# Kernel optimization log

Measured on AMD Instinct MI355X. Metric: run time of the kernel, lower is better.

## Reference

```python
import jax, jax.numpy as jnp
import numpy as np

B, T, D = 2, 2048, 1024
F_DIM = 4096
E = 8


def setup_inputs() -> dict:
    key = jax.random.key(0)
    ks = jax.random.split(key, 6)
    x = jax.random.normal(ks[0], (B, T, D), dtype=jnp.float32)
    Wr = jax.random.normal(ks[1], (E, D), dtype=jnp.float32) * 0.02  # router weight [E, D]
    W1 = jax.random.normal(ks[2], (E, F_DIM, D), dtype=jnp.float32) * 0.02  # per-expert Linear(D->F) weights
    b1 = jnp.zeros((E, F_DIM), dtype=jnp.float32)
    W2 = jax.random.normal(ks[3], (E, D, F_DIM), dtype=jnp.float32) * 0.02  # per-expert Linear(F->D) weights
    b2 = jnp.zeros((E, D), dtype=jnp.float32)
    return {"x": x, "Wr": Wr, "W1": W1, "b1": b1, "W2": W2, "b2": b2, "top_k": 2}


def reference(x, Wr, W1, b1, W2, b2, top_k):
    # router scores: [b, t, E]
    scores = jnp.einsum('btd,ed->bte', x, Wr)
    topk_vals, topk_idx = jax.lax.top_k(scores, top_k)  # [b, t, k]
    # Dense compute over all experts (E is small); grouped-GEMM equivalent of the
    # original per-token loop. hidden: [b, t, E, F]
    h = jax.nn.relu(jnp.einsum('btd,efd->btef', x, W1) + b1)
    all_out = jnp.einsum('btef,edf->bted', h, W2) + b2  # [b, t, E, D]
    # gather the top-k experts' outputs per token: [b, t, k, D]
    gathered = jnp.take_along_axis(all_out, topk_idx[..., None], axis=2)
    # FAITHFUL to source: softmax over the sequence dim (dim=-1 of [b, t]),
    # applied independently per top-k slot.
    weight = jax.nn.softmax(topk_vals, axis=1)  # [b, t, k]
    out = jnp.sum(weight[..., None] * gathered, axis=2)  # [b, t, D]
    return out
```

## Files before the change

kernel.cpp:

```cpp
#include <hip/hip_runtime.h>
#include <stdint.h>

typedef short bf16x8 __attribute__((ext_vector_type(8)));
typedef float f32x4 __attribute__((ext_vector_type(4)));

#define NTOK 4096
#define DDIM 1024
#define FDIM 4096
#define NEXP 8
#define SEQ  2048

#define FB_MAXROWS 8704
#define FB_MAXTILES 136
#define N_MAXROWS 9216
#define N_MAXTILES 72

#define GLOAD16(g, l) __builtin_amdgcn_global_load_lds( \
    (const __attribute__((address_space(1))) unsigned int*)(const void*)(g), \
    (__attribute__((address_space(3))) unsigned int*)(l), 16, 0, 0)

__device__ __forceinline__ unsigned short f2bf(float f) {
    union { float f; unsigned int u; } v; v.f = f;
    unsigned int u = v.u;
    unsigned int r = (u + 0x7FFFu + ((u >> 16) & 1u)) >> 16;
    return (unsigned short)r;
}
__device__ __forceinline__ unsigned int pk2(float a, float b) {
    return (unsigned int)f2bf(a) | ((unsigned int)f2bf(b) << 16);
}

__global__ __launch_bounds__(256) void cvt_kernel(
    const float* __restrict__ src, unsigned short* __restrict__ dst, int n4)
{
    int i = blockIdx.x * 256 + threadIdx.x;
    const int stride = gridDim.x * 256;
    for (; i < n4; i += stride) {
        const float4 v = ((const float4*)src)[i];
        ushort4 o;
        o.x = f2bf(v.x); o.y = f2bf(v.y); o.z = f2bf(v.z); o.w = f2bf(v.w);
        ((ushort4*)dst)[i] = o;
    }
}

__global__ __launch_bounds__(256) void router_kernel(
    const float* __restrict__ x, const float* __restrict__ Wr,
    float* __restrict__ topk_vals, int* __restrict__ topk_idx,
    int* __restrict__ counts)
{
    const int wave = threadIdx.x >> 6;
    const int lane = threadIdx.x & 63;
    const int t = blockIdx.x * 4 + wave;
    const float4* xr = (const float4*)(x + (size_t)t * DDIM);

    float acc[NEXP];
#pragma unroll
    for (int e = 0; e < NEXP; ++e) acc[e] = 0.0f;

    for (int d = lane; d < DDIM / 4; d += 64) {
        const float4 xv = xr[d];
#pragma unroll
        for (int e = 0; e < NEXP; ++e) {
            const float4 wv = ((const float4*)(Wr + e * DDIM))[d];
            acc[e] = fmaf(xv.x, wv.x, acc[e]);
            acc[e] = fmaf(xv.y, wv.y, acc[e]);
            acc[e] = fmaf(xv.z, wv.z, acc[e]);
            acc[e] = fmaf(xv.w, wv.w, acc[e]);
        }
    }
#pragma unroll
    for (int e = 0; e < NEXP; ++e) {
        for (int off = 32; off > 0; off >>= 1)
            acc[e] += __shfl_xor(acc[e], off, 64);
    }
    if (lane == 0) {
        float best = -3.4e38f, second = -3.4e38f;
        int bi = 0, si = 0;
#pragma unroll
        for (int e = 0; e < NEXP; ++e) {
            const float s = acc[e];
            if (s > best) { second = best; si = bi; best = s; bi = e; }
            else if (s > second) { second = s; si = e; }
        }
        topk_vals[t * 2 + 0] = best;
        topk_vals[t * 2 + 1] = second;
        topk_idx[t * 2 + 0] = bi;
        topk_idx[t * 2 + 1] = si;
        atomicAdd(&counts[bi], 1);
        atomicAdd(&counts[si], 1);
    }
}

__global__ __launch_bounds__(256) void softmax_seq_kernel(
    const float* __restrict__ tv, float* __restrict__ weight)
{
    const int b = blockIdx.x >> 1;
    const int k = blockIdx.x & 1;
    const float* base = tv + (size_t)b * SEQ * 2 + k;
    float* wbase = weight + (size_t)b * SEQ * 2 + k;
    __shared__ float red[256];
    const int tid = threadIdx.x;

    float m = -3.4e38f;
    for (int t = tid; t < SEQ; t += 256) m = fmaxf(m, base[t * 2]);
    red[tid] = m; __syncthreads();
    for (int s = 128; s > 0; s >>= 1) {
        if (tid < s) red[tid] = fmaxf(red[tid], red[tid + s]);
        __syncthreads();
    }
    m = red[0];
    __syncthreads();

    float sum = 0.0f;
    for (int t = tid; t < SEQ; t += 256) sum += expf(base[t * 2] - m);
    red[tid] = sum; __syncthreads();
    for (int s = 128; s > 0; s >>= 1) {
        if (tid < s) red[tid] += red[tid + s];
        __syncthreads();
    }
    const float inv = 1.0f / red[0];
    for (int t = tid; t < SEQ; t += 256)
        wbase[t * 2] = expf(base[t * 2] - m) * inv;
}

__global__ void scan_kernel(const int* __restrict__ counts,
                            int* __restrict__ padOff, int* __restrict__ cursor,
                            int padBits)
{
    if (threadIdx.x == 0) {
        const int pad = (1 << padBits) - 1;
        int o = 0;
        for (int e = 0; e < NEXP; ++e) {
            padOff[e] = o;
            o += ((counts[e] + pad) >> padBits) << padBits;
        }
        padOff[NEXP] = o;
    }
    if (threadIdx.x < NEXP) cursor[threadIdx.x] = 0;
}

__global__ __launch_bounds__(256) void scatter_kernel(
    const int* __restrict__ topk_idx, const int* __restrict__ padOff,
    int* __restrict__ cursor, int* __restrict__ perm)
{
    const int t = blockIdx.x * 256 + threadIdx.x;
#pragma unroll
    for (int k = 0; k < 2; ++k) {
        const int e = topk_idx[t * 2 + k];
        const int pos = padOff[e] + atomicAdd(&cursor[e], 1);
        perm[pos] = t * 2 + k;
    }
}


__global__ __launch_bounds__(256) void gemm1_n(
    const unsigned short* __restrict__ Xb, const unsigned short* __restrict__ Wb,
    const float* __restrict__ b1, const int* __restrict__ perm,
    const int* __restrict__ padOff, unsigned short* __restrict__ h)
{
    const int row0 = blockIdx.y * 128;
    if (row0 >= padOff[NEXP]) return;
    int e = 0;
#pragma unroll
    for (int i = 1; i < NEXP; ++i) if (row0 >= padOff[i]) e = i;

    __shared__ unsigned short As[128 * 64];
    __shared__ unsigned short Bs[128 * 64];

    const int tid = threadIdx.x;
    const int w = tid >> 6, lane = tid & 63;
    const int wm = (w & 1) * 64, wn = (w >> 1) * 64;
    const int fr = lane & 15, kg = lane >> 4;
    const int col0 = blockIdx.x * 128;

    const unsigned short* aSrc[4];
    const unsigned short* bSrc[4];
#pragma unroll
    for (int j = 0; j < 4; ++j) {
        const int r = w * 32 + j * 8 + (lane >> 3);
        const int pm = perm[row0 + r];
        const int tok = (pm >= 0) ? (pm >> 1) : 0;
        aSrc[j] = Xb + (size_t)tok * DDIM + (lane & 7) * 8;
        bSrc[j] = Wb + ((size_t)e * FDIM + col0 + r) * DDIM + (lane & 7) * 8;
    }

    f32x4 acc[4][4] = {};

    for (int k0 = 0; k0 < DDIM; k0 += 64) {
#pragma unroll
        for (int j = 0; j < 4; ++j) {
            GLOAD16(aSrc[j] + k0, &As[(w * 4 + j) * 512]);
            GLOAD16(bSrc[j] + k0, &Bs[(w * 4 + j) * 512]);
        }
        __syncthreads();
#pragma unroll
        for (int kk = 0; kk < 2; ++kk) {
            bf16x8 a[4], b[4];
#pragma unroll
            for (int m = 0; m < 4; ++m)
                a[m] = *(const bf16x8*)&As[(wm + m * 16 + fr) * 64 + kk * 32 + kg * 8];
#pragma unroll
            for (int n = 0; n < 4; ++n)
                b[n] = *(const bf16x8*)&Bs[(wn + n * 16 + fr) * 64 + kk * 32 + kg * 8];
#pragma unroll
            for (int m = 0; m < 4; ++m)
#pragma unroll
                for (int n = 0; n < 4; ++n)
                    acc[m][n] = __builtin_amdgcn_mfma_f32_16x16x32_bf16(a[m], b[n], acc[m][n], 0, 0, 0);
        }
        __syncthreads();
    }

#pragma unroll
    for (int n = 0; n < 4; ++n) {
        const int colg = col0 + wn + n * 16 + fr;
        const float bias = b1[e * FDIM + colg];
#pragma unroll
        for (int m = 0; m < 4; ++m) {
#pragma unroll
            for (int r = 0; r < 4; ++r) {
                const int rowg = row0 + wm + m * 16 + kg * 4 + r;
                h[(size_t)rowg * FDIM + colg] = f2bf(fmaxf(acc[m][n][r] + bias, 0.0f));
            }
        }
    }
}

__global__ __launch_bounds__(256) void gemm2_n(
    const unsigned short* __restrict__ h, const unsigned short* __restrict__ Wb,
    const float* __restrict__ b2, const int* __restrict__ perm,
    const int* __restrict__ padOff, const float* __restrict__ weight,
    float* __restrict__ out)
{
    const int row0 = blockIdx.y * 128;
    if (row0 >= padOff[NEXP]) return;
    int e = 0;
#pragma unroll
    for (int i = 1; i < NEXP; ++i) if (row0 >= padOff[i]) e = i;

    __shared__ unsigned short As[128 * 64];
    __shared__ unsigned short Bs[128 * 64];

    const int tid = threadIdx.x;
    const int w = tid >> 6, lane = tid & 63;
    const int wm = (w & 1) * 64, wn = (w >> 1) * 64;
    const int fr = lane & 15, kg = lane >> 4;
    const int col0 = blockIdx.x * 128;

    const unsigned short* aSrc[4];
    const unsigned short* bSrc[4];
#pragma unroll
    for (int j = 0; j < 4; ++j) {
        const int r = w * 32 + j * 8 + (lane >> 3);
        aSrc[j] = h + (size_t)(row0 + r) * FDIM + (lane & 7) * 8;
        bSrc[j] = Wb + ((size_t)e * DDIM + col0 + r) * FDIM + (lane & 7) * 8;
    }

    f32x4 acc[4][4] = {};

    for (int k0 = 0; k0 < FDIM; k0 += 64) {
#pragma unroll
        for (int j = 0; j < 4; ++j) {
            GLOAD16(aSrc[j] + k0, &As[(w * 4 + j) * 512]);
            GLOAD16(bSrc[j] + k0, &Bs[(w * 4 + j) * 512]);
        }
        __syncthreads();
#pragma unroll
        for (int kk = 0; kk < 2; ++kk) {
            bf16x8 a[4], b[4];
#pragma unroll
            for (int m = 0; m < 4; ++m)
                a[m] = *(const bf16x8*)&As[(wm + m * 16 + fr) * 64 + kk * 32 + kg * 8];
#pragma unroll
            for (int n = 0; n < 4; ++n)
                b[n] = *(const bf16x8*)&Bs[(wn + n * 16 + fr) * 64 + kk * 32 + kg * 8];
#pragma unroll
            for (int m = 0; m < 4; ++m)
#pragma unroll
                for (int n = 0; n < 4; ++n)
                    acc[m][n] = __builtin_amdgcn_mfma_f32_16x16x32_bf16(a[m], b[n], acc[m][n], 0, 0, 0);
        }
        __syncthreads();
    }

#pragma unroll
    for (int n = 0; n < 4; ++n) {
        const int colg = col0 + wn + n * 16 + fr;
        const float bias = b2[e * DDIM + colg];
#pragma unroll
        for (int m = 0; m < 4; ++m) {
#pragma unroll
            for (int r = 0; r < 4; ++r) {
                const int rowg = row0 + wm + m * 16 + kg * 4 + r;
                const int pm = perm[rowg];
                if (pm >= 0) {
                    const float wgt = weight[pm];
                    atomicAdd(&out[(size_t)(pm >> 1) * DDIM + colg], (acc[m][n][r] + bias) * wgt);
                }
            }
        }
    }
}


__global__ __launch_bounds__(256) void gemm1_fb(
    const float* __restrict__ x, const float* __restrict__ W1,
    const float* __restrict__ b1, const int* __restrict__ perm,
    const int* __restrict__ padOff, unsigned short* __restrict__ h)
{
    const int row0 = blockIdx.y * 64;
    if (row0 >= padOff[NEXP]) return;
    int e = 0;
#pragma unroll
    for (int i = 1; i < NEXP; ++i) if (row0 >= padOff[i]) e = i;

    __shared__ unsigned short As[64][40];
    __shared__ unsigned short Bs[64][40];

    const int tid = threadIdx.x;
    const int srow = tid >> 2;
    const int skp = (tid & 3) << 3;

    const int pm = perm[row0 + srow];
    const float* aSrc = (pm >= 0) ? (x + (size_t)(pm >> 1) * DDIM + skp) : 0;
    const int fRow = blockIdx.x * 64 + srow;
    const float* bSrc = W1 + ((size_t)e * FDIM + fRow) * DDIM + skp;

    const int lane = tid & 63;
    const int wm = ((tid >> 7) & 1) * 32;
    const int wn = ((tid >> 6) & 1) * 32;
    const int fr = lane & 15;
    const int kg = lane >> 4;

    f32x4 acc[2][2] = {{{0,0,0,0},{0,0,0,0}},{{0,0,0,0},{0,0,0,0}}};

    for (int k0 = 0; k0 < DDIM; k0 += 32) {
        uint4 av = make_uint4(0, 0, 0, 0);
        if (aSrc) {
            const float4 lo = *(const float4*)(aSrc + k0);
            const float4 hi = *(const float4*)(aSrc + k0 + 4);
            av.x = pk2(lo.x, lo.y); av.y = pk2(lo.z, lo.w);
            av.z = pk2(hi.x, hi.y); av.w = pk2(hi.z, hi.w);
        }
        const float4 bl = *(const float4*)(bSrc + k0);
        const float4 bh = *(const float4*)(bSrc + k0 + 4);
        uint4 bv;
        bv.x = pk2(bl.x, bl.y); bv.y = pk2(bl.z, bl.w);
        bv.z = pk2(bh.x, bh.y); bv.w = pk2(bh.z, bh.w);

        __syncthreads();
        *(uint4*)&As[srow][skp] = av;
        *(uint4*)&Bs[srow][skp] = bv;
        __syncthreads();

        const bf16x8 a0 = *(const bf16x8*)&As[wm + 0  + fr][kg << 3];
        const bf16x8 a1 = *(const bf16x8*)&As[wm + 16 + fr][kg << 3];
        const bf16x8 b0 = *(const bf16x8*)&Bs[wn + 0  + fr][kg << 3];
        const bf16x8 b1v = *(const bf16x8*)&Bs[wn + 16 + fr][kg << 3];
        acc[0][0] = __builtin_amdgcn_mfma_f32_16x16x32_bf16(a0, b0,  acc[0][0], 0, 0, 0);
        acc[0][1] = __builtin_amdgcn_mfma_f32_16x16x32_bf16(a0, b1v, acc[0][1], 0, 0, 0);
        acc[1][0] = __builtin_amdgcn_mfma_f32_16x16x32_bf16(a1, b0,  acc[1][0], 0, 0, 0);
        acc[1][1] = __builtin_amdgcn_mfma_f32_16x16x32_bf16(a1, b1v, acc[1][1], 0, 0, 0);
    }

#pragma unroll
    for (int mi = 0; mi < 2; ++mi)
#pragma unroll
        for (int ni = 0; ni < 2; ++ni) {
            const int colg = blockIdx.x * 64 + wn + ni * 16 + fr;
            const float bias = b1[e * FDIM + colg];
#pragma unroll
            for (int r = 0; r < 4; ++r) {
                const int rowg = row0 + wm + mi * 16 + (kg << 2) + r;
                float v = acc[mi][ni][r] + bias;
                v = fmaxf(v, 0.0f);
                h[(size_t)rowg * FDIM + colg] = f2bf(v);
            }
        }
}

__global__ __launch_bounds__(256) void gemm2_fb(
    const unsigned short* __restrict__ h, const float* __restrict__ W2,
    const float* __restrict__ b2, const int* __restrict__ perm,
    const int* __restrict__ padOff, const float* __restrict__ weight,
    float* __restrict__ out)
{
    const int row0 = blockIdx.y * 64;
    if (row0 >= padOff[NEXP]) return;
    int e = 0;
#pragma unroll
    for (int i = 1; i < NEXP; ++i) if (row0 >= padOff[i]) e = i;

    __shared__ unsigned short As[64][40];
    __shared__ unsigned short Bs[64][40];

    const int tid = threadIdx.x;
    const int srow = tid >> 2;
    const int skp = (tid & 3) << 3;

    const unsigned short* aSrc = h + (size_t)(row0 + srow) * FDIM + skp;
    const int dRow = blockIdx.x * 64 + srow;
    const float* bSrc = W2 + ((size_t)e * DDIM + dRow) * FDIM + skp;

    const int lane = tid & 63;
    const int wm = ((tid >> 7) & 1) * 32;
    const int wn = ((tid >> 6) & 1) * 32;
    const int fr = lane & 15;
    const int kg = lane >> 4;

    f32x4 acc[2][2] = {{{0,0,0,0},{0,0,0,0}},{{0,0,0,0},{0,0,0,0}}};

    for (int k0 = 0; k0 < FDIM; k0 += 32) {
        const uint4 av = *(const uint4*)(aSrc + k0);
        const float4 bl = *(const float4*)(bSrc + k0);
        const float4 bh = *(const float4*)(bSrc + k0 + 4);
        uint4 bv;
        bv.x = pk2(bl.x, bl.y); bv.y = pk2(bl.z, bl.w);
        bv.z = pk2(bh.x, bh.y); bv.w = pk2(bh.z, bh.w);

        __syncthreads();
        *(uint4*)&As[srow][skp] = av;
        *(uint4*)&Bs[srow][skp] = bv;
        __syncthreads();

        const bf16x8 a0 = *(const bf16x8*)&As[wm + 0  + fr][kg << 3];
        const bf16x8 a1 = *(const bf16x8*)&As[wm + 16 + fr][kg << 3];
        const bf16x8 b0 = *(const bf16x8*)&Bs[wn + 0  + fr][kg << 3];
        const bf16x8 b1v = *(const bf16x8*)&Bs[wn + 16 + fr][kg << 3];
        acc[0][0] = __builtin_amdgcn_mfma_f32_16x16x32_bf16(a0, b0,  acc[0][0], 0, 0, 0);
        acc[0][1] = __builtin_amdgcn_mfma_f32_16x16x32_bf16(a0, b1v, acc[0][1], 0, 0, 0);
        acc[1][0] = __builtin_amdgcn_mfma_f32_16x16x32_bf16(a1, b0,  acc[1][0], 0, 0, 0);
        acc[1][1] = __builtin_amdgcn_mfma_f32_16x16x32_bf16(a1, b1v, acc[1][1], 0, 0, 0);
    }

#pragma unroll
    for (int mi = 0; mi < 2; ++mi)
#pragma unroll
        for (int ni = 0; ni < 2; ++ni) {
            const int colg = blockIdx.x * 64 + wn + ni * 16 + fr;
            const float bias = b2[e * DDIM + colg];
#pragma unroll
            for (int r = 0; r < 4; ++r) {
                const int rowg = row0 + wm + mi * 16 + (kg << 2) + r;
                const int pm = perm[rowg];
                if (pm >= 0) {
                    const float w = weight[pm];
                    const float v = (acc[mi][ni][r] + bias) * w;
                    atomicAdd(&out[(size_t)(pm >> 1) * DDIM + colg], v);
                }
            }
        }
}

extern "C" void kernel_launch(void* const* d_in, const int* in_sizes, int n_in,
                              void* d_out, int out_size, void* d_ws, size_t ws_size,
                              hipStream_t stream)
{
    const float* x  = (const float*)d_in[0];
    const float* Wr = (const float*)d_in[1];
    const float* W1 = (const float*)d_in[2];
    const float* b1 = (const float*)d_in[3];
    const float* W2 = (const float*)d_in[4];
    const float* b2 = (const float*)d_in[5];
    float* out = (float*)d_out;
    char* ws = (char*)d_ws;

    float* topk_vals = (float*)(ws);
    float* weight    = (float*)(ws + 32768);
    int*   topk_idx  = (int*)(ws + 65536);
    int*   counts    = (int*)(ws + 98304);
    int*   padOff    = (int*)(ws + 98368);
    int*   cursor    = (int*)(ws + 98432);
    int*   perm      = (int*)(ws + 98496);

    const size_t NEED = 151257088ULL;

    if (ws_size >= NEED) {
        unsigned short* Xb = (unsigned short*)(ws + 262144);
        unsigned short* h  = (unsigned short*)(ws + 8650752);
        unsigned short* Wb = (unsigned short*)(ws + 84148224);

        hipMemsetAsync(counts, 0, NEXP * sizeof(int), stream);
        hipMemsetAsync(perm, 0xFF, N_MAXROWS * sizeof(int), stream);
        hipMemsetAsync(out, 0, (size_t)out_size * sizeof(float), stream);

        cvt_kernel<<<2048, 256, 0, stream>>>(x, Xb, NTOK * DDIM / 4);
        cvt_kernel<<<2048, 256, 0, stream>>>(W1, Wb, NEXP * FDIM * DDIM / 4);
        router_kernel<<<NTOK / 4, 256, 0, stream>>>(x, Wr, topk_vals, topk_idx, counts);
        softmax_seq_kernel<<<4, 256, 0, stream>>>(topk_vals, weight);
        scan_kernel<<<1, 64, 0, stream>>>(counts, padOff, cursor, 7);
        scatter_kernel<<<NTOK / 256, 256, 0, stream>>>(topk_idx, padOff, cursor, perm);

        gemm1_n<<<dim3(FDIM / 128, N_MAXTILES), 256, 0, stream>>>(Xb, Wb, b1, perm, padOff, h);
        cvt_kernel<<<2048, 256, 0, stream>>>(W2, Wb, NEXP * DDIM * FDIM / 4);
        gemm2_n<<<dim3(DDIM / 128, N_MAXTILES), 256, 0, stream>>>(h, Wb, b2, perm, padOff, weight, out);
    } else {
        unsigned short* h = (unsigned short*)(ws + 135168);

        hipMemsetAsync(counts, 0, NEXP * sizeof(int), stream);
        hipMemsetAsync(perm, 0xFF, FB_MAXROWS * sizeof(int), stream);
        hipMemsetAsync(out, 0, (size_t)out_size * sizeof(float), stream);

        router_kernel<<<NTOK / 4, 256, 0, stream>>>(x, Wr, topk_vals, topk_idx, counts);
        softmax_seq_kernel<<<4, 256, 0, stream>>>(topk_vals, weight);
        scan_kernel<<<1, 64, 0, stream>>>(counts, padOff, cursor, 6);
        scatter_kernel<<<NTOK / 256, 256, 0, stream>>>(topk_idx, padOff, cursor, perm);

        gemm1_fb<<<dim3(FDIM / 64, FB_MAXTILES), 256, 0, stream>>>(x, W1, b1, perm, padOff, h);
        gemm2_fb<<<dim3(DDIM / 64, FB_MAXTILES), 256, 0, stream>>>(h, W2, b2, perm, padOff, weight, out);
    }
}
```

Before: 588.4 us.

## Double-buffer LDS tiles and swizzle block order in grouped MoE GEMMs

```diff
diff --git a/kernel.cpp b/kernel.cpp
--- a/kernel.cpp
+++ b/kernel.cpp
@@ -152,25 +152,29 @@
 }
 
 
-__global__ __launch_bounds__(256) void gemm1_n(
+__global__ __launch_bounds__(256) void gemm1_p(
     const unsigned short* __restrict__ Xb, const unsigned short* __restrict__ Wb,
     const float* __restrict__ b1, const int* __restrict__ perm,
     const int* __restrict__ padOff, unsigned short* __restrict__ h)
 {
-    const int row0 = blockIdx.y * 128;
+    const int bid = blockIdx.x;
+    const int swz = (bid & 7) * (2304 / 8) + (bid >> 3);
+    const int by = swz % N_MAXTILES;
+    const int bx = swz / N_MAXTILES;
+    const int row0 = by * 128;
     if (row0 >= padOff[NEXP]) return;
     int e = 0;
 #pragma unroll
     for (int i = 1; i < NEXP; ++i) if (row0 >= padOff[i]) e = i;
 
-    __shared__ unsigned short As[128 * 64];
-    __shared__ unsigned short Bs[128 * 64];
+    __shared__ unsigned short As[2][128 * 64];
+    __shared__ unsigned short Bs[2][128 * 64];
 
     const int tid = threadIdx.x;
     const int w = tid >> 6, lane = tid & 63;
     const int wm = (w & 1) * 64, wn = (w >> 1) * 64;
     const int fr = lane & 15, kg = lane >> 4;
-    const int col0 = blockIdx.x * 128;
+    const int col0 = bx * 128;
 
     const unsigned short* aSrc[4];
     const unsigned short* bSrc[4];
@@ -185,22 +189,34 @@
 
     f32x4 acc[4][4] = {};
 
+#pragma unroll
+    for (int j = 0; j < 4; ++j) {
+        GLOAD16(aSrc[j], &As[0][(w * 4 + j) * 512]);
+        GLOAD16(bSrc[j], &Bs[0][(w * 4 + j) * 512]);
+    }
+    __syncthreads();
+
+    int cur = 0;
     for (int k0 = 0; k0 < DDIM; k0 += 64) {
-#pragma unroll
-        for (int j = 0; j < 4; ++j) {
-            GLOAD16(aSrc[j] + k0, &As[(w * 4 + j) * 512]);
-            GLOAD16(bSrc[j] + k0, &Bs[(w * 4 + j) * 512]);
-        }
-        __syncthreads();
+        const int nk = k0 + 64;
+        if (nk < DDIM) {
+#pragma unroll
+            for (int j = 0; j < 4; ++j) {
+                GLOAD16(aSrc[j] + nk, &As[cur ^ 1][(w * 4 + j) * 512]);
+                GLOAD16(bSrc[j] + nk, &Bs[cur ^ 1][(w * 4 + j) * 512]);
+            }
+        }
+        const unsigned short* Ab = &As[cur][0];
+        const unsigned short* Bb = &Bs[cur][0];
 #pragma unroll
         for (int kk = 0; kk < 2; ++kk) {
             bf16x8 a[4], b[4];
 #pragma unroll
             for (int m = 0; m < 4; ++m)
-                a[m] = *(const bf16x8*)&As[(wm + m * 16 + fr) * 64 + kk * 32 + kg * 8];
+                a[m] = *(const bf16x8*)&Ab[(wm + m * 16 + fr) * 64 + kk * 32 + kg * 8];
 #pragma unroll
             for (int n = 0; n < 4; ++n)
-                b[n] = *(const bf16x8*)&Bs[(wn + n * 16 + fr) * 64 + kk * 32 + kg * 8];
+                b[n] = *(const bf16x8*)&Bb[(wn + n * 16 + fr) * 64 + kk * 32 + kg * 8];
 #pragma unroll
             for (int m = 0; m < 4; ++m)
 #pragma unroll
@@ -208,6 +224,7 @@
                     acc[m][n] = __builtin_amdgcn_mfma_f32_16x16x32_bf16(a[m], b[n], acc[m][n], 0, 0, 0);
         }
         __syncthreads();
+        cur ^= 1;
     }
 
 #pragma unroll
@@ -225,26 +242,30 @@
     }
 }
 
-__global__ __launch_bounds__(256) void gemm2_n(
+__global__ __launch_bounds__(256) void gemm2_p(
     const unsigned short* __restrict__ h, const unsigned short* __restrict__ Wb,
     const float* __restrict__ b2, const int* __restrict__ perm,
     const int* __restrict__ padOff, const float* __restrict__ weight,
     float* __restrict__ out)
 {
-    const int row0 = blockIdx.y * 128;
+    const int bid = blockIdx.x;
+    const int swz = (bid & 7) * (576 / 8) + (bid >> 3);
+    const int by = swz % N_MAXTILES;
+    const int bx = swz / N_MAXTILES;
+    const int row0 = by * 128;
     if (row0 >= padOff[NEXP]) return;
     int e = 0;
 #pragma unroll
     for (int i = 1; i < NEXP; ++i) if (row0 >= padOff[i]) e = i;
 
-    __shared__ unsigned short As[128 * 64];
-    __shared__ unsigned short Bs[128 * 64];
+    __shared__ unsigned short As[2][128 * 64];
+    __shared__ unsigned short Bs[2][128 * 64];
 
     const int tid = threadIdx.x;
     const int w = tid >> 6, lane = tid & 63;
     const int wm = (w & 1) * 64, wn = (w >> 1) * 64;
     const int fr = lane & 15, kg = lane >> 4;
-    const int col0 = blockIdx.x * 128;
+    const int col0 = bx * 128;
 
     const unsigned short* aSrc[4];
     const unsigned short* bSrc[4];
@@ -257,22 +278,34 @@
 
     f32x4 acc[4][4] = {};
 
+#pragma unroll
+    for (int j = 0; j < 4; ++j) {
+        GLOAD16(aSrc[j], &As[0][(w * 4 + j) * 512]);
+        GLOAD16(bSrc[j], &Bs[0][(w * 4 + j) * 512]);
+    }
+    __syncthreads();
+
+    int cur = 0;
     for (int k0 = 0; k0 < FDIM; k0 += 64) {
-#pragma unroll
-        for (int j = 0; j < 4; ++j) {
-            GLOAD16(aSrc[j] + k0, &As[(w * 4 + j) * 512]);
-            GLOAD16(bSrc[j] + k0, &Bs[(w * 4 + j) * 512]);
-        }
-        __syncthreads();
+        const int nk = k0 + 64;
+        if (nk < FDIM) {
+#pragma unroll
+            for (int j = 0; j < 4; ++j) {
+                GLOAD16(aSrc[j] + nk, &As[cur ^ 1][(w * 4 + j) * 512]);
+                GLOAD16(bSrc[j] + nk, &Bs[cur ^ 1][(w * 4 + j) * 512]);
+            }
+        }
+        const unsigned short* Ab = &As[cur][0];
+        const unsigned short* Bb = &Bs[cur][0];
 #pragma unroll
         for (int kk = 0; kk < 2; ++kk) {
             bf16x8 a[4], b[4];
 #pragma unroll
             for (int m = 0; m < 4; ++m)
-                a[m] = *(const bf16x8*)&As[(wm + m * 16 + fr) * 64 + kk * 32 + kg * 8];
+                a[m] = *(const bf16x8*)&Ab[(wm + m * 16 + fr) * 64 + kk * 32 + kg * 8];
 #pragma unroll
             for (int n = 0; n < 4; ++n)
-                b[n] = *(const bf16x8*)&Bs[(wn + n * 16 + fr) * 64 + kk * 32 + kg * 8];
+                b[n] = *(const bf16x8*)&Bb[(wn + n * 16 + fr) * 64 + kk * 32 + kg * 8];
 #pragma unroll
             for (int m = 0; m < 4; ++m)
 #pragma unroll
@@ -280,6 +313,7 @@
                     acc[m][n] = __builtin_amdgcn_mfma_f32_16x16x32_bf16(a[m], b[n], acc[m][n], 0, 0, 0);
         }
         __syncthreads();
+        cur ^= 1;
     }
 
 #pragma unroll
@@ -490,9 +524,9 @@
         scan_kernel<<<1, 64, 0, stream>>>(counts, padOff, cursor, 7);
         scatter_kernel<<<NTOK / 256, 256, 0, stream>>>(topk_idx, padOff, cursor, perm);
 
-        gemm1_n<<<dim3(FDIM / 128, N_MAXTILES), 256, 0, stream>>>(Xb, Wb, b1, perm, padOff, h);
+        gemm1_p<<<32 * N_MAXTILES, 256, 0, stream>>>(Xb, Wb, b1, perm, padOff, h);
         cvt_kernel<<<2048, 256, 0, stream>>>(W2, Wb, NEXP * DDIM * FDIM / 4);
-        gemm2_n<<<dim3(DDIM / 128, N_MAXTILES), 256, 0, stream>>>(h, Wb, b2, perm, padOff, weight, out);
+        gemm2_p<<<8 * N_MAXTILES, 256, 0, stream>>>(h, Wb, b2, perm, padOff, weight, out);
     } else {
         unsigned short* h = (unsigned short*)(ws + 135168);
 
```

New measurement: 585.3 us. About the same (-0.5%).

## Use 256x256 double-buffered swizzled GEMM tiles with split-K for second expert GEMM

Applied to the files above, without the earlier changes.

```diff
diff --git a/kernel.cpp b/kernel.cpp
--- a/kernel.cpp
+++ b/kernel.cpp
@@ -12,12 +12,14 @@
 
 #define FB_MAXROWS 8704
 #define FB_MAXTILES 136
-#define N_MAXROWS 9216
-#define N_MAXTILES 72
+#define G_MAXROWS 10240
+#define G_MT 40
 
 #define GLOAD16(g, l) __builtin_amdgcn_global_load_lds( \
     (const __attribute__((address_space(1))) unsigned int*)(const void*)(g), \
     (__attribute__((address_space(3))) unsigned int*)(l), 16, 0, 0)
+
+#define SCHEDB() __builtin_amdgcn_sched_barrier(0)
 
 __device__ __forceinline__ unsigned short f2bf(float f) {
     union { float f; unsigned int u; } v; v.f = f;
@@ -152,145 +154,190 @@
 }
 
 
-__global__ __launch_bounds__(256) void gemm1_n(
+__global__ __launch_bounds__(512, 2) void gemm1_g(
     const unsigned short* __restrict__ Xb, const unsigned short* __restrict__ Wb,
     const float* __restrict__ b1, const int* __restrict__ perm,
     const int* __restrict__ padOff, unsigned short* __restrict__ h)
 {
-    const int row0 = blockIdx.y * 128;
+    const int bid = blockIdx.x;
+    const int swz = (bid & 7) * 80 + (bid >> 3);
+    const int by = swz % G_MT;
+    const int bx = swz / G_MT;
+    const int row0 = by * 256;
     if (row0 >= padOff[NEXP]) return;
     int e = 0;
 #pragma unroll
     for (int i = 1; i < NEXP; ++i) if (row0 >= padOff[i]) e = i;
 
-    __shared__ unsigned short As[128 * 64];
-    __shared__ unsigned short Bs[128 * 64];
+    __shared__ unsigned short As[2][256 * 64];
+    __shared__ unsigned short Bs[2][256 * 64];
 
     const int tid = threadIdx.x;
     const int w = tid >> 6, lane = tid & 63;
-    const int wm = (w & 1) * 64, wn = (w >> 1) * 64;
+    const int wr = (w >> 2) * 128;
+    const int wc = (w & 3) * 64;
     const int fr = lane & 15, kg = lane >> 4;
-    const int col0 = blockIdx.x * 128;
+    const int col0 = bx * 256;
+
+    const int gchunk = ((tid & 7) ^ ((tid >> 3) & 7)) * 8;
+    const int lbase = (tid >> 3) * 64 + (tid & 7) * 8;
 
     const unsigned short* aSrc[4];
     const unsigned short* bSrc[4];
 #pragma unroll
     for (int j = 0; j < 4; ++j) {
-        const int r = w * 32 + j * 8 + (lane >> 3);
+        const int r = j * 64 + (tid >> 3);
         const int pm = perm[row0 + r];
         const int tok = (pm >= 0) ? (pm >> 1) : 0;
-        aSrc[j] = Xb + (size_t)tok * DDIM + (lane & 7) * 8;
-        bSrc[j] = Wb + ((size_t)e * FDIM + col0 + r) * DDIM + (lane & 7) * 8;
-    }
-
-    f32x4 acc[4][4] = {};
-
-    for (int k0 = 0; k0 < DDIM; k0 += 64) {
-#pragma unroll
-        for (int j = 0; j < 4; ++j) {
-            GLOAD16(aSrc[j] + k0, &As[(w * 4 + j) * 512]);
-            GLOAD16(bSrc[j] + k0, &Bs[(w * 4 + j) * 512]);
-        }
-        __syncthreads();
+        aSrc[j] = Xb + (size_t)tok * DDIM + gchunk;
+        bSrc[j] = Wb + ((size_t)e * FDIM + col0 + r) * DDIM + gchunk;
+    }
+
+    f32x4 acc[8][4] = {};
+
+#define STG1(buf, koff) do { \
+    _Pragma("unroll") \
+    for (int j = 0; j < 4; ++j) { \
+        GLOAD16(aSrc[j] + (koff), &As[buf][j * 4096 + lbase]); \
+        GLOAD16(bSrc[j] + (koff), &Bs[buf][j * 4096 + lbase]); \
+    } } while (0)
+
+    const int NT = DDIM / 64;
+    STG1(0, 0);
+    __syncthreads();
+
+    int cur = 0;
+    for (int t = 0; t < NT; ++t) {
+        if (t + 1 < NT) STG1(cur ^ 1, (t + 1) * 64);
+        SCHEDB();
+        const unsigned short* Ab = &As[cur][0];
+        const unsigned short* Bb = &Bs[cur][0];
 #pragma unroll
         for (int kk = 0; kk < 2; ++kk) {
-            bf16x8 a[4], b[4];
-#pragma unroll
-            for (int m = 0; m < 4; ++m)
-                a[m] = *(const bf16x8*)&As[(wm + m * 16 + fr) * 64 + kk * 32 + kg * 8];
+            bf16x8 a[8], b[4];
+            const int cx = (((kk << 2) | kg)) ;
+#pragma unroll
+            for (int m = 0; m < 8; ++m)
+                a[m] = *(const bf16x8*)&Ab[(wr + m * 16 + fr) * 64 + ((cx ^ (fr & 7)) << 3)];
 #pragma unroll
             for (int n = 0; n < 4; ++n)
-                b[n] = *(const bf16x8*)&Bs[(wn + n * 16 + fr) * 64 + kk * 32 + kg * 8];
-#pragma unroll
-            for (int m = 0; m < 4; ++m)
+                b[n] = *(const bf16x8*)&Bb[(wc + n * 16 + fr) * 64 + ((cx ^ (fr & 7)) << 3)];
+#pragma unroll
+            for (int m = 0; m < 8; ++m)
 #pragma unroll
                 for (int n = 0; n < 4; ++n)
                     acc[m][n] = __builtin_amdgcn_mfma_f32_16x16x32_bf16(a[m], b[n], acc[m][n], 0, 0, 0);
         }
         __syncthreads();
-    }
+        cur ^= 1;
+    }
+#undef STG1
 
 #pragma unroll
     for (int n = 0; n < 4; ++n) {
-        const int colg = col0 + wn + n * 16 + fr;
+        const int colg = col0 + wc + n * 16 + fr;
         const float bias = b1[e * FDIM + colg];
 #pragma unroll
-        for (int m = 0; m < 4; ++m) {
+        for (int m = 0; m < 8; ++m) {
 #pragma unroll
             for (int r = 0; r < 4; ++r) {
-                const int rowg = row0 + wm + m * 16 + kg * 4 + r;
+                const int rowg = row0 + wr + m * 16 + kg * 4 + r;
                 h[(size_t)rowg * FDIM + colg] = f2bf(fmaxf(acc[m][n][r] + bias, 0.0f));
             }
         }
     }
 }
 
-__global__ __launch_bounds__(256) void gemm2_n(
+__global__ __launch_bounds__(512, 2) void gemm2_g(
     const unsigned short* __restrict__ h, const unsigned short* __restrict__ Wb,
     const float* __restrict__ b2, const int* __restrict__ perm,
     const int* __restrict__ padOff, const float* __restrict__ weight,
     float* __restrict__ out)
 {
-    const int row0 = blockIdx.y * 128;
+    const int bid = blockIdx.x;
+    const int swz = (bid & 7) * 80 + (bid >> 3);
+    const int by = swz % G_MT;
+    const int rest = swz / G_MT;
+    const int bx = rest & 3;
+    const int kc = rest >> 2;
+    const int row0 = by * 256;
     if (row0 >= padOff[NEXP]) return;
     int e = 0;
 #pragma unroll
     for (int i = 1; i < NEXP; ++i) if (row0 >= padOff[i]) e = i;
 
-    __shared__ unsigned short As[128 * 64];
-    __shared__ unsigned short Bs[128 * 64];
+    __shared__ unsigned short As[2][256 * 64];
+    __shared__ unsigned short Bs[2][256 * 64];
 
     const int tid = threadIdx.x;
     const int w = tid >> 6, lane = tid & 63;
-    const int wm = (w & 1) * 64, wn = (w >> 1) * 64;
+    const int wr = (w >> 2) * 128;
+    const int wc = (w & 3) * 64;
     const int fr = lane & 15, kg = lane >> 4;
-    const int col0 = blockIdx.x * 128;
+    const int col0 = bx * 256;
+    const int kbase = kc * (FDIM / 4);
+
+    const int gchunk = ((tid & 7) ^ ((tid >> 3) & 7)) * 8;
+    const int lbase = (tid >> 3) * 64 + (tid & 7) * 8;
 
     const unsigned short* aSrc[4];
     const unsigned short* bSrc[4];
 #pragma unroll
     for (int j = 0; j < 4; ++j) {
-        const int r = w * 32 + j * 8 + (lane >> 3);
-        aSrc[j] = h + (size_t)(row0 + r) * FDIM + (lane & 7) * 8;
-        bSrc[j] = Wb + ((size_t)e * DDIM + col0 + r) * FDIM + (lane & 7) * 8;
-    }
-
-    f32x4 acc[4][4] = {};
-
-    for (int k0 = 0; k0 < FDIM; k0 += 64) {
-#pragma unroll
-        for (int j = 0; j < 4; ++j) {
-            GLOAD16(aSrc[j] + k0, &As[(w * 4 + j) * 512]);
-            GLOAD16(bSrc[j] + k0, &Bs[(w * 4 + j) * 512]);
-        }
-        __syncthreads();
+        const int r = j * 64 + (tid >> 3);
+        aSrc[j] = h + (size_t)(row0 + r) * FDIM + kbase + gchunk;
+        bSrc[j] = Wb + ((size_t)e * DDIM + col0 + r) * FDIM + kbase + gchunk;
+    }
+
+    f32x4 acc[8][4] = {};
+
+#define STG2(buf, koff) do { \
+    _Pragma("unroll") \
+    for (int j = 0; j < 4; ++j) { \
+        GLOAD16(aSrc[j] + (koff), &As[buf][j * 4096 + lbase]); \
+        GLOAD16(bSrc[j] + (koff), &Bs[buf][j * 4096 + lbase]); \
+    } } while (0)
+
+    const int NT = (FDIM / 4) / 64;
+    STG2(0, 0);
+    __syncthreads();
+
+    int cur = 0;
+    for (int t = 0; t < NT; ++t) {
+        if (t + 1 < NT) STG2(cur ^ 1, (t + 1) * 64);
+        SCHEDB();
+        const unsigned short* Ab = &As[cur][0];
+        const unsigned short* Bb = &Bs[cur][0];
 #pragma unroll
         for (int kk = 0; kk < 2; ++kk) {
-            bf16x8 a[4], b[4];
-#pragma unroll
-            for (int m = 0; m < 4; ++m)
-                a[m] = *(const bf16x8*)&As[(wm + m * 16 + fr) * 64 + kk * 32 + kg * 8];
+            bf16x8 a[8], b[4];
+            const int cx = (((kk << 2) | kg));
+#pragma unroll
+            for (int m = 0; m < 8; ++m)
+                a[m] = *(const bf16x8*)&Ab[(wr + m * 16 + fr) * 64 + ((cx ^ (fr & 7)) << 3)];
 #pragma unroll
             for (int n = 0; n < 4; ++n)
-                b[n] = *(const bf16x8*)&Bs[(wn + n * 16 + fr) * 64 + kk * 32 + kg * 8];
-#pragma unroll
-            for (int m = 0; m < 4; ++m)
+                b[n] = *(const bf16x8*)&Bb[(wc + n * 16 + fr) * 64 + ((cx ^ (fr & 7)) << 3)];
+#pragma unroll
+            for (int m = 0; m < 8; ++m)
 #pragma unroll
                 for (int n = 0; n < 4; ++n)
                     acc[m][n] = __builtin_amdgcn_mfma_f32_16x16x32_bf16(a[m], b[n], acc[m][n], 0, 0, 0);
         }
         __syncthreads();
-    }
+        cur ^= 1;
+    }
+#undef STG2
 
 #pragma unroll
     for (int n = 0; n < 4; ++n) {
-        const int colg = col0 + wn + n * 16 + fr;
-        const float bias = b2[e * DDIM + colg];
-#pragma unroll
-        for (int m = 0; m < 4; ++m) {
+        const int colg = col0 + wc + n * 16 + fr;
+        const float bias = (kc == 0) ? b2[e * DDIM + colg] : 0.0f;
+#pragma unroll
+        for (int m = 0; m < 8; ++m) {
 #pragma unroll
             for (int r = 0; r < 4; ++r) {
-                const int rowg = row0 + wm + m * 16 + kg * 4 + r;
+                const int rowg = row0 + wr + m * 16 + kg * 4 + r;
                 const int pm = perm[rowg];
                 if (pm >= 0) {
                     const float wgt = weight[pm];
@@ -477,22 +524,22 @@
     if (ws_size >= NEED) {
         unsigned short* Xb = (unsigned short*)(ws + 262144);
         unsigned short* h  = (unsigned short*)(ws + 8650752);
-        unsigned short* Wb = (unsigned short*)(ws + 84148224);
+        unsigned short* Wb = (unsigned short*)(ws + 92536832);
 
         hipMemsetAsync(counts, 0, NEXP * sizeof(int), stream);
-        hipMemsetAsync(perm, 0xFF, N_MAXROWS * sizeof(int), stream);
+        hipMemsetAsync(perm, 0xFF, G_MAXROWS * sizeof(int), stream);
         hipMemsetAsync(out, 0, (size_t)out_size * sizeof(float), stream);
 
         cvt_kernel<<<2048, 256, 0, stream>>>(x, Xb, NTOK * DDIM / 4);
         cvt_kernel<<<2048, 256, 0, stream>>>(W1, Wb, NEXP * FDIM * DDIM / 4);
         router_kernel<<<NTOK / 4, 256, 0, stream>>>(x, Wr, topk_vals, topk_idx, counts);
         softmax_seq_kernel<<<4, 256, 0, stream>>>(topk_vals, weight);
-        scan_kernel<<<1, 64, 0, stream>>>(counts, padOff, cursor, 7);
+        scan_kernel<<<1, 64, 0, stream>>>(counts, padOff, cursor, 8);
         scatter_kernel<<<NTOK / 256, 256, 0, stream>>>(topk_idx, padOff, cursor, perm);
 
-        gemm1_n<<<dim3(FDIM / 128, N_MAXTILES), 256, 0, stream>>>(Xb, Wb, b1, perm, padOff, h);
+        gemm1_g<<<16 * G_MT, 512, 0, stream>>>(Xb, Wb, b1, perm, padOff, h);
         cvt_kernel<<<2048, 256, 0, stream>>>(W2, Wb, NEXP * DDIM * FDIM / 4);
-        gemm2_n<<<dim3(DDIM / 128, N_MAXTILES), 256, 0, stream>>>(h, Wb, b2, perm, padOff, weight, out);
+        gemm2_g<<<16 * G_MT, 512, 0, stream>>>(h, Wb, b2, perm, padOff, weight, out);
     } else {
         unsigned short* h = (unsigned short*)(ws + 135168);
 
```

Result: slower. 609.0 us (+3.5%).

## Swizzle LDS layout, remap block order for XCD locality, split-K second GEMM

Applied to the files above, without the earlier changes.

```diff
diff --git a/kernel.cpp b/kernel.cpp
--- a/kernel.cpp
+++ b/kernel.cpp
@@ -13,7 +13,7 @@
 #define FB_MAXROWS 8704
 #define FB_MAXTILES 136
 #define N_MAXROWS 9216
-#define N_MAXTILES 72
+#define N_MT 72
 
 #define GLOAD16(g, l) __builtin_amdgcn_global_load_lds( \
     (const __attribute__((address_space(1))) unsigned int*)(const void*)(g), \
@@ -152,12 +152,16 @@
 }
 
 
-__global__ __launch_bounds__(256) void gemm1_n(
+__global__ __launch_bounds__(256, 4) void gemm1_s(
     const unsigned short* __restrict__ Xb, const unsigned short* __restrict__ Wb,
     const float* __restrict__ b1, const int* __restrict__ perm,
     const int* __restrict__ padOff, unsigned short* __restrict__ h)
 {
-    const int row0 = blockIdx.y * 128;
+    const int bid = blockIdx.x;
+    const int swz = (bid & 7) * 288 + (bid >> 3);
+    const int by = swz % N_MT;
+    const int bx = swz / N_MT;
+    const int row0 = by * 128;
     if (row0 >= padOff[NEXP]) return;
     int e = 0;
 #pragma unroll
@@ -170,8 +174,9 @@
     const int w = tid >> 6, lane = tid & 63;
     const int wm = (w & 1) * 64, wn = (w >> 1) * 64;
     const int fr = lane & 15, kg = lane >> 4;
-    const int col0 = blockIdx.x * 128;
-
+    const int col0 = bx * 128;
+
+    const int gchunk = ((lane & 7) ^ (lane >> 3)) * 8;
     const unsigned short* aSrc[4];
     const unsigned short* bSrc[4];
 #pragma unroll
@@ -179,28 +184,31 @@
         const int r = w * 32 + j * 8 + (lane >> 3);
         const int pm = perm[row0 + r];
         const int tok = (pm >= 0) ? (pm >> 1) : 0;
-        aSrc[j] = Xb + (size_t)tok * DDIM + (lane & 7) * 8;
-        bSrc[j] = Wb + ((size_t)e * FDIM + col0 + r) * DDIM + (lane & 7) * 8;
+        aSrc[j] = Xb + (size_t)tok * DDIM + gchunk;
+        bSrc[j] = Wb + ((size_t)e * FDIM + col0 + r) * DDIM + gchunk;
     }
 
     f32x4 acc[4][4] = {};
 
-    for (int k0 = 0; k0 < DDIM; k0 += 64) {
+    const int NT = DDIM / 64;
+    for (int t = 0; t < NT; ++t) {
+        const int koff = t * 64;
 #pragma unroll
         for (int j = 0; j < 4; ++j) {
-            GLOAD16(aSrc[j] + k0, &As[(w * 4 + j) * 512]);
-            GLOAD16(bSrc[j] + k0, &Bs[(w * 4 + j) * 512]);
+            GLOAD16(aSrc[j] + koff, &As[(w * 4 + j) * 512]);
+            GLOAD16(bSrc[j] + koff, &Bs[(w * 4 + j) * 512]);
         }
         __syncthreads();
 #pragma unroll
         for (int kk = 0; kk < 2; ++kk) {
+            const int cx = (kk << 2) | kg;
             bf16x8 a[4], b[4];
 #pragma unroll
             for (int m = 0; m < 4; ++m)
-                a[m] = *(const bf16x8*)&As[(wm + m * 16 + fr) * 64 + kk * 32 + kg * 8];
+                a[m] = *(const bf16x8*)&As[(wm + m * 16 + fr) * 64 + ((cx ^ (fr & 7)) << 3)];
 #pragma unroll
             for (int n = 0; n < 4; ++n)
-                b[n] = *(const bf16x8*)&Bs[(wn + n * 16 + fr) * 64 + kk * 32 + kg * 8];
+                b[n] = *(const bf16x8*)&Bs[(wn + n * 16 + fr) * 64 + ((cx ^ (fr & 7)) << 3)];
 #pragma unroll
             for (int m = 0; m < 4; ++m)
 #pragma unroll
@@ -225,13 +233,19 @@
     }
 }
 
-__global__ __launch_bounds__(256) void gemm2_n(
+__global__ __launch_bounds__(256, 4) void gemm2_s(
     const unsigned short* __restrict__ h, const unsigned short* __restrict__ Wb,
     const float* __restrict__ b2, const int* __restrict__ perm,
     const int* __restrict__ padOff, const float* __restrict__ weight,
     float* __restrict__ out)
 {
-    const int row0 = blockIdx.y * 128;
+    const int bid = blockIdx.x;
+    const int swz = (bid & 7) * 144 + (bid >> 3);
+    const int by = swz % N_MT;
+    const int rest = swz / N_MT;
+    const int bx = rest & 7;
+    const int kc = rest >> 3;
+    const int row0 = by * 128;
     if (row0 >= padOff[NEXP]) return;
     int e = 0;
 #pragma unroll
@@ -244,35 +258,40 @@
     const int w = tid >> 6, lane = tid & 63;
     const int wm = (w & 1) * 64, wn = (w >> 1) * 64;
     const int fr = lane & 15, kg = lane >> 4;
-    const int col0 = blockIdx.x * 128;
-
+    const int col0 = bx * 128;
+    const int kbase = kc * (FDIM / 2);
+
+    const int gchunk = ((lane & 7) ^ (lane >> 3)) * 8;
     const unsigned short* aSrc[4];
     const unsigned short* bSrc[4];
 #pragma unroll
     for (int j = 0; j < 4; ++j) {
         const int r = w * 32 + j * 8 + (lane >> 3);
-        aSrc[j] = h + (size_t)(row0 + r) * FDIM + (lane & 7) * 8;
-        bSrc[j] = Wb + ((size_t)e * DDIM + col0 + r) * FDIM + (lane & 7) * 8;
+        aSrc[j] = h + (size_t)(row0 + r) * FDIM + kbase + gchunk;
+        bSrc[j] = Wb + ((size_t)e * DDIM + col0 + r) * FDIM + kbase + gchunk;
     }
 
     f32x4 acc[4][4] = {};
 
-    for (int k0 = 0; k0 < FDIM; k0 += 64) {
+    const int NT = (FDIM / 2) / 64;
+    for (int t = 0; t < NT; ++t) {
+        const int koff = t * 64;
 #pragma unroll
         for (int j = 0; j < 4; ++j) {
-            GLOAD16(aSrc[j] + k0, &As[(w * 4 + j) * 512]);
-            GLOAD16(bSrc[j] + k0, &Bs[(w * 4 + j) * 512]);
+            GLOAD16(aSrc[j] + koff, &As[(w * 4 + j) * 512]);
+            GLOAD16(bSrc[j] + koff, &Bs[(w * 4 + j) * 512]);
         }
         __syncthreads();
 #pragma unroll
         for (int kk = 0; kk < 2; ++kk) {
+            const int cx = (kk << 2) | kg;
             bf16x8 a[4], b[4];
 #pragma unroll
             for (int m = 0; m < 4; ++m)
-                a[m] = *(const bf16x8*)&As[(wm + m * 16 + fr) * 64 + kk * 32 + kg * 8];
+                a[m] = *(const bf16x8*)&As[(wm + m * 16 + fr) * 64 + ((cx ^ (fr & 7)) << 3)];
 #pragma unroll
             for (int n = 0; n < 4; ++n)
-                b[n] = *(const bf16x8*)&Bs[(wn + n * 16 + fr) * 64 + kk * 32 + kg * 8];
+                b[n] = *(const bf16x8*)&Bs[(wn + n * 16 + fr) * 64 + ((cx ^ (fr & 7)) << 3)];
 #pragma unroll
             for (int m = 0; m < 4; ++m)
 #pragma unroll
@@ -285,7 +304,7 @@
 #pragma unroll
     for (int n = 0; n < 4; ++n) {
         const int colg = col0 + wn + n * 16 + fr;
-        const float bias = b2[e * DDIM + colg];
+        const float bias = (kc == 0) ? b2[e * DDIM + colg] : 0.0f;
 #pragma unroll
         for (int m = 0; m < 4; ++m) {
 #pragma unroll
@@ -472,12 +491,12 @@
     int*   cursor    = (int*)(ws + 98432);
     int*   perm      = (int*)(ws + 98496);
 
-    const size_t NEED = 151257088ULL;
+    const size_t NEED = 159645696ULL;
 
     if (ws_size >= NEED) {
         unsigned short* Xb = (unsigned short*)(ws + 262144);
         unsigned short* h  = (unsigned short*)(ws + 8650752);
-        unsigned short* Wb = (unsigned short*)(ws + 84148224);
+        unsigned short* Wb = (unsigned short*)(ws + 92536832);
 
         hipMemsetAsync(counts, 0, NEXP * sizeof(int), stream);
         hipMemsetAsync(perm, 0xFF, N_MAXROWS * sizeof(int), stream);
@@ -490,11 +509,11 @@
         scan_kernel<<<1, 64, 0, stream>>>(counts, padOff, cursor, 7);
         scatter_kernel<<<NTOK / 256, 256, 0, stream>>>(topk_idx, padOff, cursor, perm);
 
-        gemm1_n<<<dim3(FDIM / 128, N_MAXTILES), 256, 0, stream>>>(Xb, Wb, b1, perm, padOff, h);
+        gemm1_s<<<32 * N_MT, 256, 0, stream>>>(Xb, Wb, b1, perm, padOff, h);
         cvt_kernel<<<2048, 256, 0, stream>>>(W2, Wb, NEXP * DDIM * FDIM / 4);
-        gemm2_n<<<dim3(DDIM / 128, N_MAXTILES), 256, 0, stream>>>(h, Wb, b2, perm, padOff, weight, out);
+        gemm2_s<<<16 * N_MT, 256, 0, stream>>>(h, Wb, b2, perm, padOff, weight, out);
     } else {
-        unsigned short* h = (unsigned short*)(ws + 135168);
+        unsigned short* h = (unsigned short*)(ws + 172032);
 
         hipMemsetAsync(counts, 0, NEXP * sizeof(int), stream);
         hipMemsetAsync(perm, 0xFF, FB_MAXROWS * sizeof(int), stream);
```

New measurement: 494.7 us (median of 4 runs). 15.9% less time.
